# Kernel optimization log

Hardware: AMD Instinct MI355X
Metric: run time of the kernel (lower is better)

The kernel has to match this reference:

```python
import jax, jax.numpy as jnp
import numpy as np

MODES = (32, 32)  # retained Fourier modes per spatial dim


def setup_inputs() -> dict:
    key = jax.random.key(0)
    ks = jax.random.split(key, 8)
    B, Cin, Cout, H, W = 16, 64, 64, 256, 256
    scale = 1.0 / (Cin * Cout)
    inp = {
        "x": jax.random.normal(ks[0], (B, Cin, H, W), jnp.float32),
        "t_emb": jax.random.normal(ks[1], (B, Cin), jnp.float32),
        # complex spectral weight stored as real/imag parts
        "w_real": jax.random.normal(ks[2], (Cin, Cout, *MODES), jnp.float32) * scale,
        "w_imag": jax.random.normal(ks[3], (Cin, Cout, *MODES), jnp.float32) * scale,
        # NBPFilter FiLM MLP: t_emb -> hidden(Cin) -> (gamma, beta) over Cout
        "film_w1": jax.random.normal(ks[4], (Cin, Cin), jnp.float32) / np.sqrt(Cin),
        "film_b1": jnp.zeros((Cin,), jnp.float32),
        "film_w2": jax.random.normal(ks[5], (Cin, 2 * Cout), jnp.float32) / np.sqrt(Cin),
        "film_b2": jnp.zeros((2 * Cout,), jnp.float32),
        # 1x1 conv bypass
        "bypass_w": jax.random.normal(ks[6], (Cout, Cin), jnp.float32) / np.sqrt(Cin),
        "bypass_b": jnp.zeros((Cout,), jnp.float32),
    }
    return inp


def reference(x, t_emb, w_real, w_imag, film_w1, film_b1, film_w2, film_b2, bypass_w, bypass_b):
    m0, m1 = MODES
    spatial = x.shape[-2:]
    # spectral conv: rFFT -> mode truncation -> complex einsum -> irFFT (zero-padded via s=)
    x_fft = jnp.fft.rfftn(x, axes=(-2, -1), norm="ortho")  # [B, Cin, H, W//2+1] complex
    x_fft = x_fft[:, :, :m0, :m1]                            # [B, Cin, m0, m1]
    w = w_real + 1j * w_imag                                 # [Cin, Cout, m0, m1]
    out_fft = jnp.einsum("bikl,iokl->bokl", x_fft, w)
    x_spec = jnp.fft.irfftn(out_fft, s=spatial, axes=(-2, -1), norm="ortho")  # [B, Cout, H, W]
    # NBPFilter: FiLM conditioning from t_emb
    h = jax.nn.silu(t_emb @ film_w1 + film_b1)               # [B, Cin]
    gb = h @ film_w2 + film_b2                               # [B, 2*Cout]
    gamma, beta = jnp.split(gb, 2, axis=-1)
    x_filtered = x_spec * (1.0 + gamma[:, :, None, None]) + beta[:, :, None, None]
    # 1x1 conv bypass
    byp = jnp.einsum("bihw,oi->bohw", x, bypass_w) + bypass_b[None, :, None, None]
    return jax.nn.gelu(x_filtered + byp)
```

## Files before the change

### kernel.cpp

```cpp
#include <hip/hip_runtime.h>

typedef _Float16 f16;
typedef f16 f16x8 __attribute__((ext_vector_type(8)));
typedef f16 f16x4 __attribute__((ext_vector_type(4)));
typedef f16 f16x2 __attribute__((ext_vector_type(2)));
typedef float f32x4 __attribute__((ext_vector_type(4)));

#define MFMA16(a, b, c) __builtin_amdgcn_mfma_f32_16x16x32_f16(a, b, c, 0, 0, 0)

__device__ __forceinline__ int swz(int row, int col, int width) {
    return row * width + ((((col >> 3) ^ (row & 7)) << 3) | (col & 7));
}

#define TWO_PI 6.283185307179586f
__device__ __forceinline__ float angf(int p) { return TWO_PI * (float)(p & 255) * (1.0f / 256.0f); }

__global__ __launch_bounds__(256) void prep_kernel(
    const float* __restrict__ t_emb, const float* __restrict__ film_w1,
    const float* __restrict__ film_b1, const float* __restrict__ film_w2,
    const float* __restrict__ film_b2, const float* __restrict__ bypass_b,
    const float* __restrict__ w_real, const float* __restrict__ w_imag,
    float* __restrict__ scale, float* __restrict__ bias2,
    f16* __restrict__ FmatT, f16* __restrict__ Tab2T,
    f16* __restrict__ CSTtT, f16* __restrict__ IWT, f16* __restrict__ wT)
{
    __shared__ float hbuf[16 * 64];
    int blk = blockIdx.x, t = threadIdx.x;
    if (blk < 256) {
        int k = blk >> 3, og = blk & 7;
        int i = t & 63, oq = t >> 6;
#pragma unroll
        for (int os = 0; os < 2; ++os) {
            int o = og * 8 + oq * 2 + os;
            const float* wr = w_real + ((long)(i * 64 + o) * 1024 + k * 32);
            const float* wi = w_imag + ((long)(i * 64 + o) * 1024 + k * 32);
#pragma unroll
            for (int l4 = 0; l4 < 8; ++l4) {
                float4 r = *(const float4*)(wr + l4 * 4);
                float4 m = *(const float4*)(wi + l4 * 4);
                float rv[4] = {r.x, r.y, r.z, r.w};
                float mv[4] = {m.x, m.y, m.z, m.w};
#pragma unroll
                for (int u = 0; u < 4; ++u) {
                    int l = l4 * 4 + u;
                    f16x2 p; p[0] = (f16)rv[u]; p[1] = (f16)mv[u];
                    *(f16x2*)(wT + (((long)((l * 32 + k) * 64 + o)) * 64 + i) * 2) = p;
                }
            }
        }
    } else if (blk == 256) {
        for (int r = 0; r < 4; ++r) {
            int idx = t + r * 256;
            int bb = idx >> 6, j = idx & 63;
            float acc = film_b1[j];
            for (int i = 0; i < 64; ++i) acc += t_emb[bb * 64 + i] * film_w1[i * 64 + j];
            hbuf[idx] = acc / (1.0f + __expf(-acc));
        }
        __syncthreads();
        for (int r = 0; r < 8; ++r) {
            int idx = t + r * 256;
            int bb = idx >> 7, j = idx & 127;
            float acc = film_b2[j];
            for (int i = 0; i < 64; ++i) acc += hbuf[bb * 64 + i] * film_w2[i * 128 + j];
            if (j < 64) scale[bb * 64 + j] = 1.0f + acc;
            else        bias2[bb * 64 + (j - 64)] = acc + bypass_b[j - 64];
        }
    } else {
        int bid = blk - 257;
        for (int r = 0; r < 20; ++r) {
            int e = bid * 5120 + r * 256 + t;
            float val;
            if (e < 16384) {
                int c = e >> 8, w = e & 255;
                if (c < 32) val = __cosf(angf(c * w)) * (1.0f / 256.0f);
                else        val = -__sinf(angf((c - 32) * w)) * (1.0f / 256.0f);
                FmatT[e] = (f16)val;
            } else if (e < 49152) {
                int e2 = e - 16384;
                int n = e2 >> 9, k = e2 & 511;
                int h = k & 255;
                bool first = (k < 256);
                if (n < 32) val = first ? __cosf(angf(n * h)) : __sinf(angf(n * h));
                else {
                    int m = n - 32;
                    val = first ? -__sinf(angf(m * h)) : __cosf(angf(m * h));
                }
                Tab2T[e2] = (f16)val;
            } else if (e < 65536) {
                int e2 = e - 49152;
                int h = e2 >> 6, k = e2 & 63;
                val = (k < 32) ? __cosf(angf(k * h)) : __sinf(angf((k - 32) * h));
                CSTtT[e2] = (f16)val;
            } else {
                int e2 = e - 65536;
                int w = e2 >> 6, c = e2 & 63;
                if (c == 0)      val = 1.0f / 256.0f;
                else if (c < 32) val = (2.0f / 256.0f) * __cosf(angf(c * w));
                else             val = -(2.0f / 256.0f) * __sinf(angf((c - 32) * w));
                IWT[e2] = (f16)val;
            }
        }
    }
}

__global__ __launch_bounds__(256) void k1_rowfft(
    const float* __restrict__ x, const f16* __restrict__ FmatT, f16* __restrict__ T1)
{
    __shared__ f16 A[64 * 256];
    __shared__ f16 Tr[64 * 72];
    int blk = blockIdx.x, t = threadIdx.x;
    int b = blk >> 8, ci = (blk >> 2) & 63, hc = blk & 3;
    const float* xt = x + (((long)(b * 64 + ci) * 256 + hc * 64) * 256);
    for (int j = 0; j < 16; ++j) {
        int f = j * 256 + t;
        float4 v = *(const float4*)(xt + f * 4);
        int m = f >> 6, col = (f * 4) & 255;
        f16x4 h4; h4[0] = (f16)v.x; h4[1] = (f16)v.y; h4[2] = (f16)v.z; h4[3] = (f16)v.w;
        *(f16x4*)(A + swz(m, col, 256)) = h4;
    }
    __syncthreads();
    int lane = t & 63, wv = t >> 6, kq = lane >> 4, ln = lane & 15;
    int mrow = wv * 16 + ln;
    f32x4 acc[4] = {};
    for (int ks = 0; ks < 8; ++ks) {
        int k0 = ks * 32 + kq * 8;
        f16x8 af = *(const f16x8*)(A + swz(mrow, k0, 256));
#pragma unroll
        for (int nt = 0; nt < 4; ++nt) {
            f16x8 bf = *(const f16x8*)(FmatT + (nt * 16 + ln) * 256 + k0);
            acc[nt] = MFMA16(af, bf, acc[nt]);
        }
    }
#pragma unroll
    for (int nt = 0; nt < 4; ++nt)
#pragma unroll
        for (int r = 0; r < 4; ++r) {
            int n_e = nt * 16 + ln;
            int m_e = wv * 16 + kq * 4 + r;
            Tr[n_e * 72 + m_e] = (f16)acc[nt][r];
        }
    __syncthreads();
    int c = t >> 2, q = t & 3;
    f16x8 v0 = *(const f16x8*)(Tr + c * 72 + q * 16);
    f16x8 v1 = *(const f16x8*)(Tr + c * 72 + q * 16 + 8);
    f16* dst = T1 + ((long)(b * 64 + c) * 64 + ci) * 256 + hc * 64 + q * 16;
    *(f16x8*)(dst) = v0;
    *(f16x8*)(dst + 8) = v1;
}

__global__ __launch_bounds__(256) void k2_spec(
    const f16* __restrict__ T1, const f16* __restrict__ Tab2T,
    const f16* __restrict__ wT, const f16* __restrict__ CSTtT,
    f16* __restrict__ Gmat)
{
    __shared__ union SMU {
        f16 U[64 * 512];
        struct { f16 Astk[128 * 64]; f16 Cbuf[64 * 136]; } p2;
    } sm;
    __shared__ float Xf2[64 * 64];
    int blk = blockIdx.x, t = threadIdx.x;
    int b = blk & 15, l = blk >> 4;
    const f16* pre = T1 + (long)(b * 64 + l) * 16384;
    const f16* pim = T1 + (long)(b * 64 + 32 + l) * 16384;
    for (int j = 0; j < 16; ++j) {
        int s = j * 256 + t;
        int ii = s >> 6, h = (s & 63) * 4;
        f16x4 vre = *(const f16x4*)(pre + s * 4);
        *(f16x4*)(sm.U + swz(ii, h, 512)) = vre;
        f16x4 vim = *(const f16x4*)(pim + s * 4);
        *(f16x4*)(sm.U + swz(ii, 256 + h, 512)) = vim;
    }
    __syncthreads();
    int lane = t & 63, wv = t >> 6, kq = lane >> 4, ln = lane & 15;
    {
        f32x4 acc[4] = {};
        int row = wv * 16 + ln;
        for (int ks = 0; ks < 16; ++ks) {
            int k0 = ks * 32 + kq * 8;
            f16x8 af = *(const f16x8*)(sm.U + swz(row, k0, 512));
#pragma unroll
            for (int nt = 0; nt < 4; ++nt) {
                f16x8 bf = *(const f16x8*)(Tab2T + (nt * 16 + ln) * 512 + k0);
                acc[nt] = MFMA16(af, bf, acc[nt]);
            }
        }
#pragma unroll
        for (int nt = 0; nt < 4; ++nt)
#pragma unroll
            for (int r = 0; r < 4; ++r) {
                int n_e = nt * 16 + ln;
                int i_e = wv * 16 + kq * 4 + r;
                Xf2[i_e * 64 + (n_e & 31) * 2 + (n_e >> 5)] = acc[nt][r];
            }
    }
    __syncthreads();
    {
        int o = t & 63, kg = t >> 6;
        for (int j = 0; j < 8; ++j) {
            int k = kg * 8 + j;
            const f16* wp = wT + ((long)((l * 32 + k) * 64 + o)) * 64 * 2;
            float fre = 0.0f, fim = 0.0f;
            for (int i4 = 0; i4 < 16; ++i4) {
                f16x8 w4 = *(const f16x8*)(wp + i4 * 8);
                const float* xp = Xf2 + (i4 * 4) * 64 + k * 2;
#pragma unroll
                for (int u = 0; u < 4; ++u) {
                    float xr = xp[u * 64], xi = xp[u * 64 + 1];
                    float wr = (float)w4[u * 2], wi = (float)w4[u * 2 + 1];
                    fre += xr * wr - xi * wi;
                    fim += xr * wi + xi * wr;
                }
            }
            sm.p2.Astk[swz(o,       k,      64)] = (f16)fre;
            sm.p2.Astk[swz(o,       32 + k, 64)] = (f16)(-fim);
            sm.p2.Astk[swz(64 + o,  k,      64)] = (f16)fim;
            sm.p2.Astk[swz(64 + o,  32 + k, 64)] = (f16)fre;
        }
    }
    __syncthreads();
    for (int ch = 0; ch < 4; ++ch) {
        f32x4 acc[2][4] = {};
        int rbase = wv * 32;
        for (int ks = 0; ks < 2; ++ks) {
            int k0 = ks * 32 + kq * 8;
            f16x8 bf[4];
#pragma unroll
            for (int nt = 0; nt < 4; ++nt)
                bf[nt] = *(const f16x8*)(CSTtT + (ch * 64 + nt * 16 + ln) * 64 + k0);
#pragma unroll
            for (int mi = 0; mi < 2; ++mi) {
                f16x8 af = *(const f16x8*)(sm.p2.Astk + swz(rbase + mi * 16 + ln, k0, 64));
#pragma unroll
                for (int nt = 0; nt < 4; ++nt)
                    acc[mi][nt] = MFMA16(af, bf[nt], acc[mi][nt]);
            }
        }
        __syncthreads();
#pragma unroll
        for (int mi = 0; mi < 2; ++mi)
#pragma unroll
            for (int nt = 0; nt < 4; ++nt)
#pragma unroll
                for (int r = 0; r < 4; ++r) {
                    int m_e = rbase + mi * 16 + kq * 4 + r;
                    int n_e = nt * 16 + ln;
                    sm.p2.Cbuf[n_e * 136 + m_e] = (f16)acc[mi][nt][r];
                }
        __syncthreads();
        int h_l = t >> 2, seg = t & 3;
        int h_g = ch * 64 + h_l;
        const f16* src = sm.p2.Cbuf + h_l * 136 + seg * 32;
        f16x8 a0 = *(const f16x8*)(src);
        f16x8 a1 = *(const f16x8*)(src + 8);
        f16x8 a2 = *(const f16x8*)(src + 16);
        f16x8 a3 = *(const f16x8*)(src + 24);
        f16* gd = Gmat + ((long)(b * 256 + h_g)) * 4096 + l * 64 + (seg >= 2 ? 2048 : 0) + (seg & 1) * 32;
        *(f16x8*)(gd) = a0;
        *(f16x8*)(gd + 8) = a1;
        *(f16x8*)(gd + 16) = a2;
        *(f16x8*)(gd + 24) = a3;
    }
}

__global__ __launch_bounds__(256) void k3_out(
    const float* __restrict__ x, const f16* __restrict__ Gmat,
    const f16* __restrict__ IWT, const float* __restrict__ bypass_w,
    const float* __restrict__ scale, const float* __restrict__ bias2,
    float* __restrict__ out)
{
    __shared__ f16 BT[128 * 128];
    __shared__ f16 Amat[64 * 128];
    __shared__ float biasSh[64];
    int blk = blockIdx.x, t = threadIdx.x;
    int b = blk >> 9, h = (blk >> 1) & 255, half = blk & 1;
    {
        int ipair = t >> 3, q = t & 7;
        const float* xlo = x + ((long)(b * 64 + 2 * ipair) * 256 + h) * 256 + half * 128;
        const float* xhi = xlo + 65536;
        for (int j = 0; j < 4; ++j) {
            int w4 = (q + j * 8) * 4;
            float4 lo = *(const float4*)(xlo + w4);
            float4 hi = *(const float4*)(xhi + w4);
            float lov[4] = {lo.x, lo.y, lo.z, lo.w};
            float hiv[4] = {hi.x, hi.y, hi.z, hi.w};
#pragma unroll
            for (int u = 0; u < 4; ++u) {
                f16x2 pr; pr[0] = (f16)lov[u]; pr[1] = (f16)hiv[u];
                *(f16x2*)(BT + swz(w4 + u, 2 * ipair, 128)) = pr;
            }
        }
    }
    {
        int w_l = t >> 1, cs = t & 1;
        const f16* src = IWT + (half * 128 + w_l) * 64 + cs * 32;
        for (int u = 0; u < 8; ++u) {
            f16x4 v = *(const f16x4*)(src + u * 4);
            *(f16x4*)(BT + swz(w_l, 64 + cs * 32 + u * 4, 128)) = v;
        }
    }
    {
        int o = t >> 2, s4 = t & 3;
        const float* bwp = bypass_w + o * 64 + s4 * 16;
        for (int u = 0; u < 4; ++u) {
            float4 v = *(const float4*)(bwp + u * 4);
            f16x4 hv; hv[0] = (f16)v.x; hv[1] = (f16)v.y; hv[2] = (f16)v.z; hv[3] = (f16)v.w;
            *(f16x4*)(Amat + swz(o, s4 * 16 + u * 4, 128)) = hv;
        }
    }
    {
        int c = t >> 2, s4 = t & 3;
        const f16* gp = Gmat + ((long)(b * 256 + h) * 64 + c) * 64 + s4 * 16;
        f16x8 g0 = *(const f16x8*)(gp);
        f16x8 g1 = *(const f16x8*)(gp + 8);
        float sc[16];
        for (int qq = 0; qq < 4; ++qq) {
            float4 s = *(const float4*)(scale + b * 64 + s4 * 16 + qq * 4);
            sc[qq * 4 + 0] = s.x; sc[qq * 4 + 1] = s.y; sc[qq * 4 + 2] = s.z; sc[qq * 4 + 3] = s.w;
        }
#pragma unroll
        for (int u = 0; u < 8; ++u) {
            Amat[swz(s4 * 16 + u, 64 + c, 128)] = (f16)((float)g0[u] * sc[u]);
            Amat[swz(s4 * 16 + 8 + u, 64 + c, 128)] = (f16)((float)g1[u] * sc[8 + u]);
        }
    }
    if (t < 64) biasSh[t] = bias2[b * 64 + t];
    __syncthreads();

    int lane = t & 63, wv = t >> 6, kq = lane >> 4, ln = lane & 15;
    f32x4 acc[4][2] = {};
    for (int ks = 0; ks < 4; ++ks) {
        int k0 = ks * 32 + kq * 8;
        f16x8 bf[2];
#pragma unroll
        for (int nt = 0; nt < 2; ++nt)
            bf[nt] = *(const f16x8*)(BT + swz(wv * 32 + nt * 16 + ln, k0, 128));
#pragma unroll
        for (int mt = 0; mt < 4; ++mt) {
            f16x8 af = *(const f16x8*)(Amat + swz(mt * 16 + ln, k0, 128));
#pragma unroll
            for (int nt = 0; nt < 2; ++nt)
                acc[mt][nt] = MFMA16(af, bf[nt], acc[mt][nt]);
        }
    }
    long obase = ((long)(b * 64) * 256 + h) * 256 + half * 128;
#pragma unroll
    for (int mt = 0; mt < 4; ++mt)
#pragma unroll
        for (int nt = 0; nt < 2; ++nt)
#pragma unroll
            for (int r = 0; r < 4; ++r) {
                int o = mt * 16 + kq * 4 + r;
                int n = wv * 32 + nt * 16 + ln;
                float v = acc[mt][nt][r] + biasSh[o];
                float uu = 0.7978845608028654f * (v + 0.044715f * v * v * v);
                float e = __expf(2.0f * uu);
                float th = 1.0f - 2.0f / (e + 1.0f);
                out[obase + (long)o * 65536 + n] = 0.5f * v * (1.0f + th);
            }
}

extern "C" void kernel_launch(void* const* d_in, const int* in_sizes, int n_in,
                              void* d_out, int out_size, void* d_ws, size_t ws_size,
                              hipStream_t stream) {
    const float* x        = (const float*)d_in[0];
    const float* t_emb    = (const float*)d_in[1];
    const float* w_real   = (const float*)d_in[2];
    const float* w_imag   = (const float*)d_in[3];
    const float* film_w1  = (const float*)d_in[4];
    const float* film_b1  = (const float*)d_in[5];
    const float* film_w2  = (const float*)d_in[6];
    const float* film_b2  = (const float*)d_in[7];
    const float* bypass_w = (const float*)d_in[8];
    const float* bypass_b = (const float*)d_in[9];
    float* out = (float*)d_out;
    char* ws = (char*)d_ws;

    float* scale = (float*)(ws + 0);
    float* bias2 = (float*)(ws + 4096);
    f16* FmatT = (f16*)(ws + 8192);
    f16* Tab2T = (f16*)(ws + 40960);
    f16* CSTtT = (f16*)(ws + 106496);
    f16* IWT   = (f16*)(ws + 139264);
    f16* wT    = (f16*)(ws + 172032);
    f16* T1    = (f16*)(ws + 16949248);
    f16* Gmat  = (f16*)(ws + 50503680);

    hipLaunchKernelGGL(prep_kernel, dim3(273), dim3(256), 0, stream,
                       t_emb, film_w1, film_b1, film_w2, film_b2, bypass_b,
                       w_real, w_imag, scale, bias2, FmatT, Tab2T, CSTtT, IWT, wT);
    hipLaunchKernelGGL(k1_rowfft, dim3(4096), dim3(256), 0, stream, x, FmatT, T1);
    hipLaunchKernelGGL(k2_spec, dim3(512), dim3(256), 0, stream, T1, Tab2T, wT, CSTtT, Gmat);
    hipLaunchKernelGGL(k3_out, dim3(8192), dim3(256), 0, stream, x, Gmat, IWT,
                       bypass_w, scale, bias2, out);
}
```

Baseline: 684.2 us.

## Move weight transpose into row-FFT kernel, remap blocks for XCD locality, nontemporal output stores

Moves the spectral-weight f16 transpose out of the prep kernel and into extra blocks of the row-FFT kernel, so the prep launch shrinks to 17 blocks and the transpose overlaps with FFT work. k2 and k3 block indices are remapped so blocks sharing data land on the same XCD or neighbouring rows, aiming for better L2 locality. k2's inner complex MAC loop now reads float2 pairs with partial unrolling, and the final output uses nontemporal stores so the large result does not pollute the cache. The weight-transpose blocks add load imbalance to k1, and the remappings assume a round-robin dispatch across XCDs.

```diff
diff --git a/kernel.cpp b/kernel.cpp
--- a/kernel.cpp
+++ b/kernel.cpp
@@ -19,36 +19,13 @@
     const float* __restrict__ t_emb, const float* __restrict__ film_w1,
     const float* __restrict__ film_b1, const float* __restrict__ film_w2,
     const float* __restrict__ film_b2, const float* __restrict__ bypass_b,
-    const float* __restrict__ w_real, const float* __restrict__ w_imag,
     float* __restrict__ scale, float* __restrict__ bias2,
     f16* __restrict__ FmatT, f16* __restrict__ Tab2T,
-    f16* __restrict__ CSTtT, f16* __restrict__ IWT, f16* __restrict__ wT)
+    f16* __restrict__ CSTtT, f16* __restrict__ IWT)
 {
     __shared__ float hbuf[16 * 64];
     int blk = blockIdx.x, t = threadIdx.x;
-    if (blk < 256) {
-        int k = blk >> 3, og = blk & 7;
-        int i = t & 63, oq = t >> 6;
-#pragma unroll
-        for (int os = 0; os < 2; ++os) {
-            int o = og * 8 + oq * 2 + os;
-            const float* wr = w_real + ((long)(i * 64 + o) * 1024 + k * 32);
-            const float* wi = w_imag + ((long)(i * 64 + o) * 1024 + k * 32);
-#pragma unroll
-            for (int l4 = 0; l4 < 8; ++l4) {
-                float4 r = *(const float4*)(wr + l4 * 4);
-                float4 m = *(const float4*)(wi + l4 * 4);
-                float rv[4] = {r.x, r.y, r.z, r.w};
-                float mv[4] = {m.x, m.y, m.z, m.w};
-#pragma unroll
-                for (int u = 0; u < 4; ++u) {
-                    int l = l4 * 4 + u;
-                    f16x2 p; p[0] = (f16)rv[u]; p[1] = (f16)mv[u];
-                    *(f16x2*)(wT + (((long)((l * 32 + k) * 64 + o)) * 64 + i) * 2) = p;
-                }
-            }
-        }
-    } else if (blk == 256) {
+    if (blk == 0) {
         for (int r = 0; r < 4; ++r) {
             int idx = t + r * 256;
             int bb = idx >> 6, j = idx & 63;
@@ -66,7 +43,7 @@
             else        bias2[bb * 64 + (j - 64)] = acc + bypass_b[j - 64];
         }
     } else {
-        int bid = blk - 257;
+        int bid = blk - 1;
         for (int r = 0; r < 20; ++r) {
             int e = bid * 5120 + r * 256 + t;
             float val;
@@ -104,12 +81,39 @@
 }
 
 __global__ __launch_bounds__(256) void k1_rowfft(
-    const float* __restrict__ x, const f16* __restrict__ FmatT, f16* __restrict__ T1)
+    const float* __restrict__ x, const f16* __restrict__ FmatT, f16* __restrict__ T1,
+    const float* __restrict__ w_real, const float* __restrict__ w_imag,
+    f16* __restrict__ wT)
 {
     __shared__ f16 A[64 * 256];
     __shared__ f16 Tr[64 * 72];
     int blk = blockIdx.x, t = threadIdx.x;
-    int b = blk >> 8, ci = (blk >> 2) & 63, hc = blk & 3;
+    if (blk < 256) {
+        int k = blk >> 3, og = blk & 7;
+        int i = t & 63, oq = t >> 6;
+#pragma unroll
+        for (int os = 0; os < 2; ++os) {
+            int o = og * 8 + oq * 2 + os;
+            const float* wr = w_real + ((long)(i * 64 + o) * 1024 + k * 32);
+            const float* wi = w_imag + ((long)(i * 64 + o) * 1024 + k * 32);
+#pragma unroll
+            for (int l4 = 0; l4 < 8; ++l4) {
+                float4 r = *(const float4*)(wr + l4 * 4);
+                float4 m = *(const float4*)(wi + l4 * 4);
+                float rv[4] = {r.x, r.y, r.z, r.w};
+                float mv[4] = {m.x, m.y, m.z, m.w};
+#pragma unroll
+                for (int u = 0; u < 4; ++u) {
+                    int l = l4 * 4 + u;
+                    f16x2 p; p[0] = (f16)rv[u]; p[1] = (f16)mv[u];
+                    *(f16x2*)(wT + (((long)((l * 32 + k) * 64 + o)) * 64 + i) * 2) = p;
+                }
+            }
+        }
+        return;
+    }
+    int kb = blk - 256;
+    int b = kb >> 8, ci = (kb >> 2) & 63, hc = kb & 3;
     const float* xt = x + (((long)(b * 64 + ci) * 256 + hc * 64) * 256);
     for (int j = 0; j < 16; ++j) {
         int f = j * 256 + t;
@@ -159,7 +163,8 @@
     } sm;
     __shared__ float Xf2[64 * 64];
     int blk = blockIdx.x, t = threadIdx.x;
-    int b = blk & 15, l = blk >> 4;
+    int xcd = blk & 7, i2 = blk >> 3;
+    int l = xcd * 4 + (i2 & 3), b = i2 >> 2;
     const f16* pre = T1 + (long)(b * 64 + l) * 16384;
     const f16* pim = T1 + (long)(b * 64 + 32 + l) * 16384;
     for (int j = 0; j < 16; ++j) {
@@ -199,16 +204,17 @@
         for (int j = 0; j < 8; ++j) {
             int k = kg * 8 + j;
             const f16* wp = wT + ((long)((l * 32 + k) * 64 + o)) * 64 * 2;
+            const float2* xp2 = (const float2*)(Xf2 + k * 2);
             float fre = 0.0f, fim = 0.0f;
+#pragma unroll 4
             for (int i4 = 0; i4 < 16; ++i4) {
                 f16x8 w4 = *(const f16x8*)(wp + i4 * 8);
-                const float* xp = Xf2 + (i4 * 4) * 64 + k * 2;
 #pragma unroll
                 for (int u = 0; u < 4; ++u) {
-                    float xr = xp[u * 64], xi = xp[u * 64 + 1];
+                    float2 xv = xp2[(i4 * 4 + u) * 32];
                     float wr = (float)w4[u * 2], wi = (float)w4[u * 2 + 1];
-                    fre += xr * wr - xi * wi;
-                    fim += xr * wi + xi * wr;
+                    fre += xv.x * wr - xv.y * wi;
+                    fim += xv.x * wi + xv.y * wr;
                 }
             }
             sm.p2.Astk[swz(o,       k,      64)] = (f16)fre;
@@ -272,7 +278,10 @@
     __shared__ f16 Amat[64 * 128];
     __shared__ float biasSh[64];
     int blk = blockIdx.x, t = threadIdx.x;
-    int b = blk >> 9, h = (blk >> 1) & 255, half = blk & 1;
+    int g = blk >> 4, rr = blk & 15;
+    int half = rr >> 3;
+    int pair = g * 8 + (rr & 7);
+    int b = pair >> 8, h = pair & 255;
     {
         int ipair = t >> 3, q = t & 7;
         const float* xlo = x + ((long)(b * 64 + 2 * ipair) * 256 + h) * 256 + half * 128;
@@ -355,7 +364,8 @@
                 float uu = 0.7978845608028654f * (v + 0.044715f * v * v * v);
                 float e = __expf(2.0f * uu);
                 float th = 1.0f - 2.0f / (e + 1.0f);
-                out[obase + (long)o * 65536 + n] = 0.5f * v * (1.0f + th);
+                __builtin_nontemporal_store(0.5f * v * (1.0f + th),
+                                            &out[obase + (long)o * 65536 + n]);
             }
 }
 
@@ -385,10 +395,11 @@
     f16* T1    = (f16*)(ws + 16949248);
     f16* Gmat  = (f16*)(ws + 50503680);
 
-    hipLaunchKernelGGL(prep_kernel, dim3(273), dim3(256), 0, stream,
+    hipLaunchKernelGGL(prep_kernel, dim3(17), dim3(256), 0, stream,
                        t_emb, film_w1, film_b1, film_w2, film_b2, bypass_b,
-                       w_real, w_imag, scale, bias2, FmatT, Tab2T, CSTtT, IWT, wT);
-    hipLaunchKernelGGL(k1_rowfft, dim3(4096), dim3(256), 0, stream, x, FmatT, T1);
+                       scale, bias2, FmatT, Tab2T, CSTtT, IWT);
+    hipLaunchKernelGGL(k1_rowfft, dim3(4352), dim3(256), 0, stream, x, FmatT, T1,
+                       w_real, w_imag, wT);
     hipLaunchKernelGGL(k2_spec, dim3(512), dim3(256), 0, stream, T1, Tab2T, wT, CSTtT, Gmat);
     hipLaunchKernelGGL(k3_out, dim3(8192), dim3(256), 0, stream, x, Gmat, IWT,
                        bypass_w, scale, bias2, out);
```

Measured after the change: 676.6 us. About the same (-1.1%).
